# Kernel tuning notes

Hardware: AMD Instinct MI355X
Metric: run time of the kernel (lower is better)

Reference implementation:

```python
import jax, jax.numpy as jnp
import numpy as np

N_SERIES = 100000
INPUT_SIZE = 28
OUTPUT_SIZE = 7
N_T = 1
N_S = 4
PERIOD = 7            # seasonality = [7]
EMBED = 1 + 1 + PERIOD  # lev_sms, seas_sms, init seasonal factors
BATCH = 2048
N_TIME = 2048


def setup_inputs() -> dict:
    key = jax.random.key(0)
    k1, k2, k3, k4 = jax.random.split(key, 4)
    # Y must be strictly positive (multiplicative model: division + log)
    Y = jax.random.uniform(k1, (BATCH, N_TIME), dtype=jnp.float32, minval=0.5, maxval=1.5)
    X = jax.random.normal(k2, (BATCH, N_T, N_TIME), dtype=jnp.float32)
    S = jax.random.normal(k3, (BATCH, N_S), dtype=jnp.float32)
    idxs = jax.random.randint(k4, (BATCH,), 0, N_SERIES)
    embeds_weight = jnp.full((N_SERIES, EMBED), 0.5, dtype=jnp.float32)
    return {"S": S, "Y": Y, "X": X, "idxs": idxs,
            "embeds_weight": embeds_weight, "step_size": 7}


def _levels_seasons(Y, idxs, embeds_weight):
    """Exponential smoothing level/seasonality recurrence (single seasonality)."""
    emb = embeds_weight[idxs]                      # (B, 9)
    lev_sms = jax.nn.sigmoid(emb[:, 0])            # (B,)
    seas_sms = jax.nn.sigmoid(emb[:, 1])           # (B,)
    init_seas = jnp.exp(emb[:, 2:2 + PERIOD])      # (B, 7)

    level0 = Y[:, 0] / init_seas[:, 0]
    # ring buffer holding the seasonal factors used at steps t=1..: [s1..s6, s0]
    buf0 = jnp.concatenate([init_seas[:, 1:], init_seas[:, :1]], axis=1)  # (B, 7)

    def step(carry, inp):
        lev, buf = carry
        y, k = inp
        s = jnp.take(buf, k % PERIOD, axis=1)                       # seasonality at lag PERIOD
        newlev = lev_sms * (y / s) + (1.0 - lev_sms) * lev
        news = seas_sms * (y / newlev) + (1.0 - seas_sms) * s
        buf = jax.lax.dynamic_update_slice_in_dim(buf, news[:, None], k % PERIOD, axis=1)
        return (newlev, buf), (newlev, news)

    ks = jnp.arange(N_TIME - 1, dtype=jnp.int32)
    (_, _), (levs, seas) = jax.lax.scan(step, (level0, buf0), (Y[:, 1:].T, ks))
    levels = jnp.concatenate([level0[:, None], levs.T], axis=1)           # (B, n_time)
    seasonal = jnp.concatenate([init_seas, init_seas[:, :1], seas.T], axis=1)  # (B, n_time+7)
    return levels, seasonal


def reference(S, Y, X, idxs, embeds_weight, step_size):
    levels, seasonal = _levels_seasons(Y, idxs, embeds_weight)

    windows_end = N_TIME - INPUT_SIZE - OUTPUT_SIZE + 1
    windows = np.arange(0, windows_end, step_size)          # static window starts
    W = len(windows)

    # --- insample windows, normalized: log(Y / level / season) ---
    idx_in = windows[:, None] + np.arange(INPUT_SIZE)       # (W, I)
    Yw = Y[:, idx_in]                                       # (B, W, I)
    lev_w = levels[:, windows + INPUT_SIZE - 1]             # (B, W)
    seas_w = seasonal[:, idx_in]                            # (B, W, I)
    y_in = jnp.log(Yw / (lev_w[:, :, None] * seas_w))
    y_in = y_in.transpose(1, 0, 2)                          # (W, B, I)

    # --- exogenous windows: X[:, :, start:start+I+O].reshape(B, -1) ---
    idx_x = windows[:, None] + np.arange(INPUT_SIZE + OUTPUT_SIZE)  # (W, I+O)
    Xw = X[:, :, idx_x].transpose(2, 0, 1, 3).reshape(W, BATCH, N_T * (INPUT_SIZE + OUTPUT_SIZE))

    # --- static features ---
    Sw = jnp.broadcast_to(S[None], (W, BATCH, N_S))

    windows_y_insample = jnp.concatenate([y_in, Xw, Sw], axis=2)   # (W, B, context)

    # --- outsample windows (eval mode: not normalized) ---
    idx_out = windows[:, None] + INPUT_SIZE + np.arange(OUTPUT_SIZE)  # (W, O)
    windows_y_outsample = Y[:, idx_out].transpose(1, 0, 2)            # (W, B, O)

    return windows_y_insample, windows_y_outsample, levels, seasonal
```

## Files before the change

### kernel.cpp

```cpp
#include <hip/hip_runtime.h>
#include <math.h>

#define BATCH 2048
#define N_TIME 2048
#define INPUT_SIZE 28
#define OUTPUT_SIZE 7
#define N_S 4
#define PERIOD 7
#define EMBED 9
#define SEAS_LEN (N_TIME + PERIOD)
#define W_COUNT 288
#define WB_COUNT (W_COUNT * BATCH)
#define INS_COLS 67
#define OUT0_SIZE (WB_COUNT * INS_COLS)
#define OUT1_SIZE (WB_COUNT * OUTPUT_SIZE)
#define LEV_SIZE (BATCH * N_TIME)
#define SEAS_SIZE (BATCH * SEAS_LEN)

#define M0_COPY (WB_COUNT * 39)
#define M_COPY  (M0_COPY + OUT1_SIZE)
#define COPY_BLOCKS 480
#define GRID1 (32 + COPY_BLOCKS)
#define N_YIN (WB_COUNT * INPUT_SIZE)
#define CUNROLL 16

struct ScanState {
    float lev, lsms, seas_sms, oma, oms;
    float sbuf[PERIOD];
    float rbuf[PERIOD];
    float yp, sp, rnlp, rnsp;
};

template<bool FIRST, bool LAST, bool PREF>
__device__ __forceinline__ void scan_chunk(
    int base, int l,
    const float* __restrict__ Yb,
    float (&cur)[64], float (&nxt)[64],
    float (*__restrict__ tl)[65], float (*__restrict__ ts)[65],
    ScanState& st)
{
    if (PREF) {
#pragma unroll
        for (int k = 0; k < 64; k += 4)
            *(float4*)&nxt[k] = *(const float4*)(Yb + base + 64 + k);
    }
    tl[l][0] = st.lev;
#pragma unroll
    for (int k = 0; k < 64; ++k) {
        if (!LAST || k < 63) {
            float y  = (k < 63) ? cur[k + 1] : nxt[0];
            float s0 = st.sbuf[0];
            float nl = fmaf(st.oma, st.lev, y * st.rbuf[0]);
            st.lev = nl;
            tl[l][k + 1] = nl;
            if (!FIRST || k > 0) {
                float u  = st.yp * st.rnlp;
                float ns = fmaf(st.oms, st.sp, st.seas_sms * u);
                ts[l][k] = ns;
                st.sbuf[PERIOD - 1] = ns;
                if (!FIRST || k > 1)
                    st.rbuf[PERIOD - 2] = st.lsms * st.rnsp;
                st.rnsp = __builtin_amdgcn_rcpf(ns);
            }
            float rnl = __builtin_amdgcn_rcpf(nl);
#pragma unroll
            for (int q = 0; q < PERIOD - 1; ++q) st.sbuf[q] = st.sbuf[q + 1];
#pragma unroll
            for (int q = 0; q < PERIOD - 1; ++q) st.rbuf[q] = st.rbuf[q + 1];
            st.yp = y; st.sp = s0; st.rnlp = rnl;
        }
    }
    if (LAST) {
        float u  = st.yp * st.rnlp;
        float ns = fmaf(st.oms, st.sp, st.seas_sms * u);
        ts[l][63] = ns;
    }
    asm volatile("s_waitcnt lgkmcnt(0)" ::: "memory");
    __builtin_amdgcn_s_barrier();
}

__device__ __forceinline__ void drain_chunk(
    int base, int jr, int km, int r0,
    const float (*__restrict__ tl)[65], const float (*__restrict__ ts)[65],
    float* __restrict__ levels, float* __restrict__ seasonal)
{
    __builtin_amdgcn_s_barrier();
    asm volatile("" ::: "memory");
#pragma unroll
    for (int j0 = 0; j0 < 64; j0 += 4) {
        int j = j0 + jr;
        float vl[4], vs[4];
#pragma unroll
        for (int i = 0; i < 4; ++i) { vl[i] = tl[j][km + i]; vs[i] = ts[j][km + i]; }
        float4 v4; v4.x = vl[0]; v4.y = vl[1]; v4.z = vl[2]; v4.w = vl[3];
        *(float4*)(levels + (size_t)(r0 + j) * N_TIME + base + km) = v4;
        float* srow = seasonal + (size_t)(r0 + j) * SEAS_LEN + base + 7 + km;
#pragma unroll
        for (int i = 0; i < 4; ++i) srow[i] = vs[i];
    }
    asm volatile("s_waitcnt lgkmcnt(0)" ::: "memory");
}

__device__ __forceinline__ void copy_addr(
    unsigned g,
    const float* __restrict__ Y, const float* __restrict__ X,
    const float* __restrict__ S,
    float* __restrict__ out0, float* __restrict__ out1,
    const float*& src, float*& dst)
{
    if (g < M0_COPY) {
        unsigned wb = g / 39u;
        int jj = (int)(g - wb * 39u);
        int w  = (int)(wb >> 11);
        int b  = (int)(wb & (BATCH - 1));
        src = (jj < 35) ? &X[b * N_TIME + w * 7 + jj]
                        : &S[b * N_S + (jj - 35)];
        dst = &out0[(size_t)wb * 67u + 28u + (unsigned)jj];
    } else {
        unsigned e  = g - M0_COPY;
        unsigned wb = e / 7u;
        int m  = (int)(e - wb * 7u);
        int w  = (int)(wb >> 11);
        int b  = (int)(wb & (BATCH - 1));
        src = &Y[b * N_TIME + w * 7 + INPUT_SIZE + m];
        dst = &out1[e];
    }
}

__global__ __launch_bounds__(128, 1) void es_scan_plus(
    const float* __restrict__ Y, const int* __restrict__ idxs,
    const float* __restrict__ emb, const float* __restrict__ X,
    const float* __restrict__ S,
    float* __restrict__ levels, float* __restrict__ seasonal,
    float* __restrict__ out0, float* __restrict__ out1)
{
    __shared__ float tl[2][64][65];
    __shared__ float ts[2][64][65];
    const int tid = threadIdx.x;
    const int l   = tid & 63;

    if (blockIdx.x >= 32) {
        const unsigned stride = COPY_BLOCKS * 128;
        unsigned g = (blockIdx.x - 32) * 128 + tid;
#pragma unroll 1
        for (; g + (CUNROLL - 1) * stride < M_COPY; g += stride * CUNROLL) {
            const float* src[CUNROLL]; float* dst[CUNROLL]; float v[CUNROLL];
#pragma unroll
            for (int u = 0; u < CUNROLL; ++u)
                copy_addr(g + (unsigned)u * stride, Y, X, S, out0, out1, src[u], dst[u]);
#pragma unroll
            for (int u = 0; u < CUNROLL; ++u) v[u] = *src[u];
#pragma unroll
            for (int u = 0; u < CUNROLL; ++u) *dst[u] = v[u];
        }
#pragma unroll 1
        for (; g < M_COPY; g += stride) {
            const float* src; float* dst;
            copy_addr(g, Y, X, S, out0, out1, src, dst);
            *dst = *src;
        }
        return;
    }

    const int r0 = blockIdx.x * 64;
    if (tid < 64) {
        const int b = r0 + l;
        const float* Yb = Y + (size_t)b * N_TIME;
        const float* e  = emb + (size_t)idxs[b] * EMBED;
        ScanState st;
        st.lsms     = 1.0f / (1.0f + __expf(-e[0]));
        st.seas_sms = 1.0f / (1.0f + __expf(-e[1]));
        st.oma = 1.0f - st.lsms;
        st.oms = 1.0f - st.seas_sms;
        float is[PERIOD];
#pragma unroll
        for (int j = 0; j < PERIOD; ++j) is[j] = __expf(e[2 + j]);
        st.lev = Yb[0] / is[0];

        float* seab = seasonal + (size_t)b * SEAS_LEN;
#pragma unroll
        for (int j = 0; j < PERIOD; ++j) seab[j] = is[j];
        ts[0][l][0] = is[0];
#pragma unroll
        for (int j = 0; j < PERIOD; ++j) st.sbuf[j] = is[(j + 1) % PERIOD];
#pragma unroll
        for (int j = 0; j < PERIOD; ++j)
            st.rbuf[j] = st.lsms * __builtin_amdgcn_rcpf(st.sbuf[j]);
        st.yp = 0.0f; st.sp = 1.0f; st.rnlp = 1.0f; st.rnsp = 1.0f;

        float ya[64], yb2[64];
#pragma unroll
        for (int k = 0; k < 64; k += 4)
            *(float4*)&ya[k] = *(const float4*)(Yb + k);

        scan_chunk<true,  false, true >(0, l, Yb, ya, yb2, tl[0], ts[0], st);
#pragma unroll 1
        for (int cc = 0; cc < 15; ++cc) {
            scan_chunk<false, false, true>(64  + cc * 128, l, Yb, yb2, ya, tl[1], ts[1], st);
            scan_chunk<false, false, true>(128 + cc * 128, l, Yb, ya, yb2, tl[0], ts[0], st);
        }
        scan_chunk<false, true,  false>(1984, l, Yb, yb2, ya, tl[1], ts[1], st);
    } else {
        const int jr = l >> 4;
        const int km = (l & 15) * 4;
#pragma unroll 1
        for (int c = 0; c < 32; ++c)
            drain_chunk(c * 64, jr, km, r0, tl[c & 1], ts[c & 1], levels, seasonal);
    }
}

__global__ __launch_bounds__(256) void es_windows_yin(
    const float* __restrict__ Y, const float* __restrict__ levels,
    const float* __restrict__ seasonal, float* __restrict__ out0)
{
    unsigned gid = blockIdx.x * 256 + threadIdx.x;
    unsigned wb = gid / 28u;
    int j  = (int)(gid - wb * 28u);
    int w  = (int)(wb >> 11);
    int b  = (int)(wb & (BATCH - 1));
    int t0 = w * 7;
    float y  = Y[b * N_TIME + t0 + j];
    float lv = levels[b * N_TIME + t0 + INPUT_SIZE - 1];
    float sv = seasonal[b * SEAS_LEN + t0 + j];
    out0[(size_t)wb * 67u + (unsigned)j] =
        __logf(y * __builtin_amdgcn_rcpf(lv * sv));
}

extern "C" void kernel_launch(void* const* d_in, const int* in_sizes, int n_in,
                              void* d_out, int out_size, void* d_ws, size_t ws_size,
                              hipStream_t stream) {
    const float* S    = (const float*)d_in[0];
    const float* Y    = (const float*)d_in[1];
    const float* X    = (const float*)d_in[2];
    const int*   idxs = (const int*)d_in[3];
    const float* emb  = (const float*)d_in[4];

    float* out      = (float*)d_out;
    float* out_ins  = out;
    float* out_outs = out + OUT0_SIZE;
    float* levels   = out + OUT0_SIZE + OUT1_SIZE;
    float* seasonal = out + OUT0_SIZE + OUT1_SIZE + LEV_SIZE;

    es_scan_plus<<<GRID1, 128, 0, stream>>>(
        Y, idxs, emb, X, S, levels, seasonal, out_ins, out_outs);

    es_windows_yin<<<N_YIN / 256, 256, 0, stream>>>(
        Y, levels, seasonal, out_ins);
}
```

Measured before the change: 349.1 us.

## Fuse y_in window kernel into scan kernel with flag-gated work stealing

Removes the separate y_in window kernel. Each scan block publishes a release flag once its 64 series' levels and seasonals are written. Copy blocks and finished scan blocks then pull chunks of y_in work per super-batch through an atomic counter, after acquiring that flag. This aims to overlap y_in computation with the long serial scan and to avoid a second launch and its tail. In exchange it adds a memset, spin-waiting on flags, and a dependency on all 512 blocks being co-resident, which could deadlock if they are not.

Result: slower. 481.5 us (+37.9%).

```diff
diff --git a/kernel.cpp b/kernel.cpp
--- a/kernel.cpp
+++ b/kernel.cpp
@@ -21,8 +21,11 @@
 #define M_COPY  (M0_COPY + OUT1_SIZE)
 #define COPY_BLOCKS 480
 #define GRID1 (32 + COPY_BLOCKS)
-#define N_YIN (WB_COUNT * INPUT_SIZE)
 #define CUNROLL 16
+
+#define YIN_PER_SB (W_COUNT * 64 * INPUT_SIZE)
+#define YIN_CHUNK  (128 * INPUT_SIZE)
+#define YIN_CHUNKS_PER_SB (YIN_PER_SB / YIN_CHUNK)
 
 struct ScanState {
     float lev, lsms, seas_sms, oma, oms;
@@ -127,15 +130,67 @@
     }
 }
 
+__device__ __forceinline__ void yin_chunk_do(
+    int sb, int c, int tid,
+    const float* __restrict__ Y, const float* __restrict__ levels,
+    const float* __restrict__ seasonal, float* __restrict__ out0)
+{
+    int base = c * YIN_CHUNK;
+#pragma unroll
+    for (int k = 0; k < INPUT_SIZE; ++k) {
+        unsigned e    = (unsigned)(base + k * 128 + tid);
+        unsigned w    = e / 1792u;
+        unsigned rem  = e - w * 1792u;
+        unsigned brel = rem / 28u;
+        unsigned j    = rem - brel * 28u;
+        int b  = sb * 64 + (int)brel;
+        int t0 = (int)w * 7;
+        float y  = Y[b * N_TIME + t0 + (int)j];
+        float lv = levels[b * N_TIME + t0 + INPUT_SIZE - 1];
+        float sv = seasonal[b * SEAS_LEN + t0 + (int)j];
+        size_t wb = (size_t)w * BATCH + (size_t)b;
+        out0[wb * 67u + j] = __logf(y * __builtin_amdgcn_rcpf(lv * sv));
+    }
+}
+
+__device__ __forceinline__ void yin_steal(
+    int tid, int sb0, int* __restrict__ flags, int* __restrict__ qc,
+    int* s_chunk,
+    const float* __restrict__ Y, const float* __restrict__ levels,
+    const float* __restrict__ seasonal, float* __restrict__ out0)
+{
+#pragma unroll 1
+    for (int i = 0; i < 32; ++i) {
+        int sb = (sb0 + i) & 31;
+        if (tid == 0) {
+            while (__hip_atomic_load(&flags[sb], __ATOMIC_ACQUIRE,
+                                     __HIP_MEMORY_SCOPE_AGENT) == 0)
+                __builtin_amdgcn_s_sleep(32);
+        }
+        __syncthreads();
+#pragma unroll 1
+        for (;;) {
+            if (tid == 0) *s_chunk = atomicAdd(&qc[sb * 16], 1);
+            __syncthreads();
+            int c = *s_chunk;
+            __syncthreads();
+            if (c >= YIN_CHUNKS_PER_SB) break;
+            yin_chunk_do(sb, c, tid, Y, levels, seasonal, out0);
+        }
+    }
+}
+
 __global__ __launch_bounds__(128, 1) void es_scan_plus(
     const float* __restrict__ Y, const int* __restrict__ idxs,
     const float* __restrict__ emb, const float* __restrict__ X,
     const float* __restrict__ S,
     float* __restrict__ levels, float* __restrict__ seasonal,
-    float* __restrict__ out0, float* __restrict__ out1)
+    float* __restrict__ out0, float* __restrict__ out1,
+    int* __restrict__ flags, int* __restrict__ qc)
 {
     __shared__ float tl[2][64][65];
     __shared__ float ts[2][64][65];
+    __shared__ int s_chunk;
     const int tid = threadIdx.x;
     const int l   = tid & 63;
 
@@ -159,6 +214,8 @@
             copy_addr(g, Y, X, S, out0, out1, src, dst);
             *dst = *src;
         }
+        yin_steal(tid, (int)(blockIdx.x & 31), flags, qc, &s_chunk,
+                  Y, levels, seasonal, out0);
         return;
     }
 
@@ -176,10 +233,6 @@
 #pragma unroll
         for (int j = 0; j < PERIOD; ++j) is[j] = __expf(e[2 + j]);
         st.lev = Yb[0] / is[0];
-
-        float* seab = seasonal + (size_t)b * SEAS_LEN;
-#pragma unroll
-        for (int j = 0; j < PERIOD; ++j) seab[j] = is[j];
         ts[0][l][0] = is[0];
 #pragma unroll
         for (int j = 0; j < PERIOD; ++j) st.sbuf[j] = is[(j + 1) % PERIOD];
@@ -201,29 +254,26 @@
         }
         scan_chunk<false, true,  false>(1984, l, Yb, yb2, ya, tl[1], ts[1], st);
     } else {
+        const int b = r0 + l;
+        {
+            const float* e = emb + (size_t)idxs[b] * EMBED;
+            float* seab = seasonal + (size_t)b * SEAS_LEN;
+#pragma unroll
+            for (int j = 0; j < PERIOD; ++j) seab[j] = __expf(e[2 + j]);
+        }
         const int jr = l >> 4;
         const int km = (l & 15) * 4;
 #pragma unroll 1
         for (int c = 0; c < 32; ++c)
             drain_chunk(c * 64, jr, km, r0, tl[c & 1], ts[c & 1], levels, seasonal);
-    }
-}
-
-__global__ __launch_bounds__(256) void es_windows_yin(
-    const float* __restrict__ Y, const float* __restrict__ levels,
-    const float* __restrict__ seasonal, float* __restrict__ out0)
-{
-    unsigned gid = blockIdx.x * 256 + threadIdx.x;
-    unsigned wb = gid / 28u;
-    int j  = (int)(gid - wb * 28u);
-    int w  = (int)(wb >> 11);
-    int b  = (int)(wb & (BATCH - 1));
-    int t0 = w * 7;
-    float y  = Y[b * N_TIME + t0 + j];
-    float lv = levels[b * N_TIME + t0 + INPUT_SIZE - 1];
-    float sv = seasonal[b * SEAS_LEN + t0 + j];
-    out0[(size_t)wb * 67u + (unsigned)j] =
-        __logf(y * __builtin_amdgcn_rcpf(lv * sv));
+        asm volatile("s_waitcnt vmcnt(0)" ::: "memory");
+        if (l == 0)
+            __hip_atomic_store(&flags[blockIdx.x], 1, __ATOMIC_RELEASE,
+                               __HIP_MEMORY_SCOPE_AGENT);
+    }
+    __syncthreads();
+    yin_steal(tid, (int)blockIdx.x, flags, qc, &s_chunk,
+              Y, levels, seasonal, out0);
 }
 
 extern "C" void kernel_launch(void* const* d_in, const int* in_sizes, int n_in,
@@ -241,9 +291,11 @@
     float* levels   = out + OUT0_SIZE + OUT1_SIZE;
     float* seasonal = out + OUT0_SIZE + OUT1_SIZE + LEV_SIZE;
 
+    int* flags = (int*)d_ws;
+    int* qc    = flags + 32;
+
+    hipMemsetAsync(d_ws, 0, (32 + 32 * 16) * sizeof(int), stream);
+
     es_scan_plus<<<GRID1, 128, 0, stream>>>(
-        Y, idxs, emb, X, S, levels, seasonal, out_ins, out_outs);
-
-    es_windows_yin<<<N_YIN / 256, 256, 0, stream>>>(
-        Y, levels, seasonal, out_ins);
-}
+        Y, idxs, emb, X, S, levels, seasonal, out_ins, out_outs, flags, qc);
+}
```
